# Kernel optimization log

Hardware: AMD Instinct MI355X
Metric: run time of the kernel (lower is better)

Reference implementation:

```python
import math
import jax, jax.numpy as jnp
import numpy as np

NLAT, NLON = 61, 120
C, H = 64, 4
DH = C // H
HID = 128
NSEG = NLAT * NLON  # number of grid points / softmax segments
EPS = 1e-6
SCALE = 1.0 / math.sqrt(DH)


def _build_geometry():
    """Neighbor pairs within theta_cutoff on the equiangular (pole-including) grid.

    The neighborhood structure is longitude-shift invariant, so we enumerate it
    for output longitude 0 and replicate with a modular longitude shift.
    """
    nlat, nlon = NLAT, NLON
    theta = np.pi * np.arange(nlat) / (nlat - 1)           # colatitudes incl. poles
    lam = 2.0 * np.pi * np.arange(nlon) / nlon
    theta_cutoff = 7.0 / math.sqrt(math.pi) * math.pi / (nlat - 1)
    ct, st = np.cos(theta), np.sin(theta)
    # great-circle distance between (theta_o, 0) and (theta_i, dlon): [nlat, nlat, nlon]
    cosd = (ct[:, None, None] * ct[None, :, None]
            + st[:, None, None] * st[None, :, None] * np.cos(lam)[None, None, :])
    dist = np.arccos(np.clip(cosd, -1.0, 1.0))
    ho, hi, dl = np.nonzero(dist <= theta_cutoff)          # E reference-column entries
    wo = np.arange(nlon)
    out_idx = (ho[:, None] * nlon + wo[None, :]).reshape(-1).astype(np.int32)
    in_idx = (hi[:, None] * nlon + (dl[:, None] + wo[None, :]) % nlon).reshape(-1).astype(np.int32)
    # quadrature (integration) weights: sin(theta) measure, zero at the poles
    w = (st * (np.pi / (nlat - 1)) * (2.0 * np.pi / nlon)).astype(np.float32)
    quad_w = np.repeat(w, nlon)                            # [NSEG]
    return jnp.asarray(out_idx), jnp.asarray(in_idx), jnp.asarray(quad_w)


def setup_inputs() -> dict:
    key = jax.random.key(0)
    ks = jax.random.split(key, 8)
    out_idx, in_idx, quad_w = _build_geometry()

    def w(k, shape, fan_in):
        return jax.random.normal(k, shape, dtype=jnp.float32) / np.float32(np.sqrt(fan_in))

    return {
        "x": jax.random.normal(ks[0], (1, C, NLAT, NLON), dtype=jnp.float32),
        "wq": w(ks[1], (C, C), C),
        "wk": w(ks[2], (C, C), C),
        "wv": w(ks[3], (C, C), C),
        "wo": w(ks[4], (C, C), C),
        "w1": w(ks[5], (HID, C), C),
        "b1": jnp.zeros((HID,), jnp.float32),
        "w2": w(ks[6], (C, HID), HID),
        "b2": jnp.zeros((C,), jnp.float32),
        "ln0_g": jnp.ones((C,), jnp.float32),
        "ln0_b": jnp.zeros((C,), jnp.float32),
        "ln1_g": jnp.ones((C,), jnp.float32),
        "ln1_b": jnp.zeros((C,), jnp.float32),
        "quad_w": quad_w,
        "out_idx": out_idx,
        "in_idx": in_idx,
    }


def _layernorm(x, g, b):
    # channel-wise LayerNorm at every spatial location; x: [B, C, H, W]
    m = jnp.mean(x, axis=1, keepdims=True)
    v = jnp.mean((x - m) ** 2, axis=1, keepdims=True)
    xh = (x - m) * jax.lax.rsqrt(v + EPS)
    return xh * g[None, :, None, None] + b[None, :, None, None]


def _neighborhood_attn(x, wq, wk, wv, wo, quad_w, out_idx, in_idx):
    # x: [B, C, nlat, nlon] (fp32)
    B = x.shape[0]
    q = jnp.einsum('oc,bchw->bohw', wq, x).reshape(B, H, DH, NSEG)
    k = jnp.einsum('oc,bchw->bohw', wk, x).reshape(B, H, DH, NSEG)
    v = jnp.einsum('oc,bchw->bohw', wv, x).reshape(B, H, DH, NSEG)
    qg = q[..., out_idx]                                   # [B,H,DH,NNZ]
    kg = k[..., in_idx]
    s = jnp.einsum('bhdn,bhdn->bhn', qg, kg) * SCALE       # [B,H,NNZ]
    s = jnp.moveaxis(s, -1, 0)                             # [NNZ,B,H]
    smax = jax.ops.segment_max(s, out_idx, num_segments=NSEG)
    # quadrature-weighted, numerically stable softmax over each neighborhood
    alpha = jnp.exp(s - smax[out_idx]) * quad_w[in_idx][:, None, None]
    vg = jnp.moveaxis(v[..., in_idx], -1, 0)               # [NNZ,B,H,DH]
    num = jax.ops.segment_sum(alpha[..., None] * vg, out_idx, num_segments=NSEG)
    den = jax.ops.segment_sum(alpha, out_idx, num_segments=NSEG)
    att = num / den[..., None]                             # [NSEG,B,H,DH]
    att = jnp.moveaxis(att, 0, -1).reshape(B, C, NLAT, NLON)
    return jnp.einsum('oc,bchw->bohw', wo, att)


def reference(x, wq, wk, wv, wo, w1, b1, w2, b2, ln0_g, ln0_b, ln1_g, ln1_b,
              quad_w, out_idx, in_idx):
    residual = x
    h0 = _layernorm(x, ln0_g, ln0_b)
    a = _neighborhood_attn(h0.astype(jnp.float32), wq, wk, wv, wo,
                           quad_w, out_idx, in_idx).astype(x.dtype)
    x1 = a + residual
    h1 = _layernorm(x1, ln1_g, ln1_b)
    m = jax.nn.gelu(jnp.einsum('fc,bchw->bfhw', w1, h1) + b1[None, :, None, None],
                    approximate=False)
    m = jnp.einsum('cf,bfhw->bchw', w2, m) + b2[None, :, None, None]
    return m + x1
```

## Files before the change

### kernel.cpp

```cpp
#include <hip/hip_runtime.h>
#include <math.h>

#define NSEG 7320
#define NLON 120
#define HIDN 128
#define ECH  16
#define MAXCH 48

__global__ __launch_bounds__(64) void k1_ln_qkv(
    const float* __restrict__ x,  const float* __restrict__ wq,
    const float* __restrict__ wk, const float* __restrict__ wv,
    const float* __restrict__ g,  const float* __restrict__ b,
    const int* __restrict__ out_idx, const int* __restrict__ in_idx,
    const float* __restrict__ qw, int E,
    float* __restrict__ q_pl, float* __restrict__ k_pl, float* __restrict__ v_pl,
    int* __restrict__ row_start, int4* __restrict__ meta,
    float4* __restrict__ zbase)
{
    const int lane = threadIdx.x;
    const int tile = blockIdx.x;
    const int grp  = blockIdx.y;

    if (grp >= 25) {
        const int n4 = (68 * NSEG) / 4;
        for (int i = ((grp - 25) * 115 + tile) * 64 + lane; i < n4; i += 2 * 115 * 64)
            zbase[i] = make_float4(0.f, 0.f, 0.f, 0.f);
        return;
    }
    if (grp == 24) {
        for (int e = tile * 64 + lane; e < E; e += 115 * 64) {
            int ho = out_idx[e * NLON] / NLON;
            if (e == 0) {
                row_start[ho] = 0;
            } else {
                int hp = out_idx[(e - 1) * NLON] / NLON;
                if (hp != ho) row_start[ho] = e;
            }
            if (e == E - 1) row_start[ho + 1] = E;
            int i0 = in_idx[e * NLON];
            int hi = i0 / NLON;
            int dl = i0 - hi * NLON;
            meta[e] = make_int4(hi * NLON, dl, __float_as_int(qw[i0]), ho);
        }
        return;
    }

    const int n = tile * 64 + lane;
    if (n >= NSEG) return;

    float xv[64];
    float s = 0.f, s2 = 0.f;
#pragma unroll
    for (int c = 0; c < 64; ++c) { float t = x[c * NSEG + n]; xv[c] = t; s += t; s2 += t * t; }
    float mean = s * 0.015625f;
    float var  = s2 * 0.015625f - mean * mean;
    float rstd = rsqrtf(var + 1e-6f);
#pragma unroll
    for (int c = 0; c < 64; ++c) xv[c] = (xv[c] - mean) * rstd * g[c] + b[c];

    const int mm    = grp >> 3;
    const int obase = (grp & 7) * 8;
    const float* __restrict__ w = (mm == 0) ? wq : (mm == 1) ? wk : wv;
    float* __restrict__ dst = (mm == 0) ? q_pl : (mm == 1) ? k_pl : v_pl;
    const float scale = (mm == 0) ? 0.25f : 1.0f;

#pragma unroll
    for (int j = 0; j < 8; ++j) {
        int o = obase + j;
        float acc = 0.f;
#pragma unroll
        for (int c = 0; c < 64; ++c) acc += w[o * 64 + c] * xv[c];
        dst[o * NSEG + n] = acc * scale;
    }
}

__global__ __launch_bounds__(128) void k2_attn(
    const float* __restrict__ q_pl, const float* __restrict__ k_pl,
    const float* __restrict__ v_pl,
    const int4* __restrict__ meta,  const int* __restrict__ row_start,
    float* __restrict__ num, float* __restrict__ den)
{
    const int wo  = threadIdx.x;
    const bool aw = wo < NLON;
    const int woc = aw ? wo : (NLON - 1);
    const int ho  = blockIdx.x;
    const int head = blockIdx.z;
    const int cb  = head * 16;

    int e0 = __builtin_amdgcn_readfirstlane(row_start[ho]);
    int e1 = __builtin_amdgcn_readfirstlane(row_start[ho + 1]);
    int eb = e0 + blockIdx.y * ECH;
    if (eb >= e1) return;
    int ee = eb + ECH; if (ee > e1) ee = e1;

    const int segc = ho * NLON + woc;
    const float* __restrict__ qb = q_pl + (size_t)cb * NSEG;
    const float* __restrict__ kb = k_pl + (size_t)cb * NSEG;
    const float* __restrict__ vb = v_pl + (size_t)cb * NSEG;

    float qreg[16];
#pragma unroll
    for (int c = 0; c < 16; ++c) qreg[c] = qb[c * NSEG + segc];

    float acc[16];
#pragma unroll
    for (int c = 0; c < 16; ++c) acc[c] = 0.f;
    float dh = 0.f;

#pragma unroll 2
    for (int e = eb; e < ee; ++e) {
        int4 mt = meta[e];
        int dlw = mt.y + woc; if (dlw >= NLON) dlw -= NLON;
        const float* __restrict__ kp = kb + (mt.x + dlw);
        const float* __restrict__ vp = vb + (mt.x + dlw);

        float sa = 0.f, sb = 0.f;
#pragma unroll
        for (int c = 0; c < 8; ++c)  sa += qreg[c]     * kp[c * NSEG];
#pragma unroll
        for (int c = 0; c < 8; ++c)  sb += qreg[8 + c] * kp[(8 + c) * NSEG];

        float qwv = aw ? __int_as_float(mt.z) : 0.f;
        float a = __expf(sa + sb) * qwv;
        dh += a;

#pragma unroll
        for (int c = 0; c < 16; ++c) acc[c] = fmaf(a, vp[c * NSEG], acc[c]);
    }

    if (aw) {
        const int seg = ho * NLON + wo;
#pragma unroll
        for (int c = 0; c < 16; ++c) atomicAdd(&num[(cb + c) * NSEG + seg], acc[c]);
        atomicAdd(&den[head * NSEG + seg], dh);
    }
}

__global__ __launch_bounds__(64) void k2c_wo(
    const float* __restrict__ num, const float* __restrict__ den,
    const float* __restrict__ wo,  const float* __restrict__ x,
    float* __restrict__ x1)
{
    const int lane = threadIdx.x;
    const int n    = blockIdx.x * 64 + lane;
    if (n >= NSEG) return;

    float rdh[4];
#pragma unroll
    for (int h = 0; h < 4; ++h) rdh[h] = 1.0f / den[h * NSEG + n];

    float att[64];
#pragma unroll
    for (int c = 0; c < 64; ++c) att[c] = num[c * NSEG + n] * rdh[c >> 4];

    const int o0 = blockIdx.y * 8;
#pragma unroll
    for (int j = 0; j < 8; ++j) {
        int o = o0 + j;
        float acc = 0.f;
#pragma unroll
        for (int c = 0; c < 64; ++c) acc += wo[o * 64 + c] * att[c];
        x1[o * NSEG + n] = acc + x[o * NSEG + n];
    }
}

__global__ __launch_bounds__(64) void k3a_mlp1(
    const float* __restrict__ x1, const float* __restrict__ w1,
    const float* __restrict__ b1, const float* __restrict__ g,
    const float* __restrict__ bb, float* __restrict__ m_act)
{
    const int lane = threadIdx.x;
    const int n    = blockIdx.x * 64 + lane;
    if (n >= NSEG) return;

    float xv[64];
    float s = 0.f, s2 = 0.f;
#pragma unroll
    for (int c = 0; c < 64; ++c) { float t = x1[c * NSEG + n]; xv[c] = t; s += t; s2 += t * t; }
    float mean = s * 0.015625f;
    float var  = s2 * 0.015625f - mean * mean;
    float rstd = rsqrtf(var + 1e-6f);
#pragma unroll
    for (int c = 0; c < 64; ++c) xv[c] = (xv[c] - mean) * rstd * g[c] + bb[c];

    const int h0 = blockIdx.y * 8;
#pragma unroll
    for (int j = 0; j < 8; ++j) {
        int h = h0 + j;
        float mh = b1[h];
#pragma unroll
        for (int c = 0; c < 64; ++c) mh += w1[h * 64 + c] * xv[c];
        m_act[h * NSEG + n] = 0.5f * mh * (1.0f + erff(mh * 0.70710678118654752f));
    }
}

__global__ __launch_bounds__(64) void k3b_mlp2(
    const float* __restrict__ m_act, const float* __restrict__ w2,
    const float* __restrict__ b2,    const float* __restrict__ x1,
    float* __restrict__ out)
{
    const int lane = threadIdx.x;
    const int n    = blockIdx.x * 64 + lane;
    if (n >= NSEG) return;
    const int c0   = blockIdx.y * 8;

    float acc[8];
#pragma unroll
    for (int j = 0; j < 8; ++j) acc[j] = 0.f;

#pragma unroll 8
    for (int h = 0; h < HIDN; ++h) {
        float mh = m_act[h * NSEG + n];
#pragma unroll
        for (int j = 0; j < 8; ++j) acc[j] += w2[(c0 + j) * HIDN + h] * mh;
    }
#pragma unroll
    for (int j = 0; j < 8; ++j) {
        int c = c0 + j;
        out[c * NSEG + n] = acc[j] + b2[c] + x1[c * NSEG + n];
    }
}

extern "C" void kernel_launch(void* const* d_in, const int* in_sizes, int n_in,
                              void* d_out, int out_size, void* d_ws, size_t ws_size,
                              hipStream_t stream)
{
    const float* x    = (const float*)d_in[0];
    const float* wq   = (const float*)d_in[1];
    const float* wk   = (const float*)d_in[2];
    const float* wv   = (const float*)d_in[3];
    const float* wo   = (const float*)d_in[4];
    const float* w1   = (const float*)d_in[5];
    const float* b1   = (const float*)d_in[6];
    const float* w2   = (const float*)d_in[7];
    const float* b2   = (const float*)d_in[8];
    const float* ln0g = (const float*)d_in[9];
    const float* ln0b = (const float*)d_in[10];
    const float* ln1g = (const float*)d_in[11];
    const float* ln1b = (const float*)d_in[12];
    const float* qw   = (const float*)d_in[13];
    const int* out_idx = (const int*)d_in[14];
    const int* in_idx  = (const int*)d_in[15];
    float* out = (float*)d_out;

    const int NNZ = in_sizes[15];
    const int E   = NNZ / NLON;
    const size_t N64 = (size_t)NSEG * 64;

    float* ws    = (float*)d_ws;
    float* q_pl  = ws;
    float* k_pl  = ws + N64;
    float* v_pl  = ws + 2 * N64;
    float* num   = ws + 3 * N64;
    float* den   = ws + 4 * N64;
    float* x1    = ws + 4 * N64 + 4 * NSEG;
    float* m_act = ws + 5 * N64 + 4 * NSEG;
    int*   row_start = (int*)(ws + 7 * N64 + 4 * NSEG);
    int4*  meta  = (int4*)(ws + 7 * N64 + 4 * NSEG + 64);

    hipLaunchKernelGGL(k1_ln_qkv, dim3(115, 27), dim3(64), 0, stream,
                       x, wq, wk, wv, ln0g, ln0b, out_idx, in_idx, qw, E,
                       q_pl, k_pl, v_pl, row_start, meta, (float4*)num);
    hipLaunchKernelGGL(k2_attn, dim3(61, MAXCH, 4), dim3(128), 0, stream,
                       q_pl, k_pl, v_pl, meta, row_start, num, den);
    hipLaunchKernelGGL(k2c_wo, dim3(115, 8), dim3(64), 0, stream,
                       num, den, wo, x, x1);
    hipLaunchKernelGGL(k3a_mlp1, dim3(115, 16), dim3(64), 0, stream,
                       x1, w1, b1, ln1g, ln1b, m_act);
    hipLaunchKernelGGL(k3b_mlp2, dim3(115, 8), dim3(64), 0, stream,
                       m_act, w2, b2, x1, out);
}
```

Before: 186.8 us.

## Replace attention atomics with per-chunk partial buffers and a separate reduction kernel

The attention kernel now writes each edge-chunk's partial numerator and denominator to a dedicated slice of a partial buffer instead of issuing atomicAdds into num/den. A new reduction kernel sums the valid chunks per row, which also removes the need to zero num/den inside the first kernel. The edge chunk size is doubled and the chunk count halved, so there are fewer blocks and fewer partial slices to reduce. This avoids atomic contention and the zeroing pass, at the cost of an extra kernel launch and extra global memory traffic for the partials.

```diff
diff --git a/kernel.cpp b/kernel.cpp
--- a/kernel.cpp
+++ b/kernel.cpp
@@ -4,8 +4,8 @@
 #define NSEG 7320
 #define NLON 120
 #define HIDN 128
-#define ECH  16
-#define MAXCH 48
+#define ECH  32
+#define MAXCH 24
 
 __global__ __launch_bounds__(64) void k1_ln_qkv(
     const float* __restrict__ x,  const float* __restrict__ wq,
@@ -14,19 +14,12 @@
     const int* __restrict__ out_idx, const int* __restrict__ in_idx,
     const float* __restrict__ qw, int E,
     float* __restrict__ q_pl, float* __restrict__ k_pl, float* __restrict__ v_pl,
-    int* __restrict__ row_start, int4* __restrict__ meta,
-    float4* __restrict__ zbase)
+    int* __restrict__ row_start, int4* __restrict__ meta)
 {
     const int lane = threadIdx.x;
     const int tile = blockIdx.x;
     const int grp  = blockIdx.y;
 
-    if (grp >= 25) {
-        const int n4 = (68 * NSEG) / 4;
-        for (int i = ((grp - 25) * 115 + tile) * 64 + lane; i < n4; i += 2 * 115 * 64)
-            zbase[i] = make_float4(0.f, 0.f, 0.f, 0.f);
-        return;
-    }
     if (grp == 24) {
         for (int e = tile * 64 + lane; e < E; e += 115 * 64) {
             int ho = out_idx[e * NLON] / NLON;
@@ -78,18 +71,19 @@
     const float* __restrict__ q_pl, const float* __restrict__ k_pl,
     const float* __restrict__ v_pl,
     const int4* __restrict__ meta,  const int* __restrict__ row_start,
-    float* __restrict__ num, float* __restrict__ den)
+    float* __restrict__ part)
 {
     const int wo  = threadIdx.x;
     const bool aw = wo < NLON;
     const int woc = aw ? wo : (NLON - 1);
     const int ho  = blockIdx.x;
+    const int j   = blockIdx.y;
     const int head = blockIdx.z;
     const int cb  = head * 16;
 
     int e0 = __builtin_amdgcn_readfirstlane(row_start[ho]);
     int e1 = __builtin_amdgcn_readfirstlane(row_start[ho + 1]);
-    int eb = e0 + blockIdx.y * ECH;
+    int eb = e0 + j * ECH;
     if (eb >= e1) return;
     int ee = eb + ECH; if (ee > e1) ee = e1;
 
@@ -130,10 +124,42 @@
 
     if (aw) {
         const int seg = ho * NLON + wo;
-#pragma unroll
-        for (int c = 0; c < 16; ++c) atomicAdd(&num[(cb + c) * NSEG + seg], acc[c]);
-        atomicAdd(&den[head * NSEG + seg], dh);
-    }
+        float* __restrict__ pb = part + ((size_t)j * 68) * NSEG;
+#pragma unroll
+        for (int c = 0; c < 16; ++c)
+            pb[(cb + c) * NSEG + seg] = acc[c];
+        pb[(64 + head) * NSEG + seg] = dh;
+    }
+}
+
+__global__ __launch_bounds__(64) void k2r_reduce(
+    const float* __restrict__ part, const int* __restrict__ row_start,
+    float* __restrict__ num, float* __restrict__ den)
+{
+    const int lane = threadIdx.x;
+    const int n    = blockIdx.x * 64 + lane;
+    if (n >= NSEG) return;
+    const int c    = blockIdx.y;
+    const int row  = n / NLON;
+    const int len  = row_start[row + 1] - row_start[row];
+    const int nch  = (len + ECH - 1) / ECH;
+
+    const float* __restrict__ pb = part + (size_t)c * NSEG + n;
+    const size_t jst = (size_t)68 * NSEG;
+
+    float s0 = 0.f, s1 = 0.f, s2 = 0.f, s3 = 0.f;
+    int j = 0;
+    for (; j + 4 <= nch; j += 4) {
+        s0 += pb[(size_t)j * jst];
+        s1 += pb[(size_t)(j + 1) * jst];
+        s2 += pb[(size_t)(j + 2) * jst];
+        s3 += pb[(size_t)(j + 3) * jst];
+    }
+    for (; j < nch; ++j) s0 += pb[(size_t)j * jst];
+    float s = (s0 + s1) + (s2 + s3);
+
+    if (c < 64) num[c * NSEG + n] = s;
+    else        den[(c - 64) * NSEG + n] = s;
 }
 
 __global__ __launch_bounds__(64) void k2c_wo(
@@ -257,12 +283,15 @@
     float* m_act = ws + 5 * N64 + 4 * NSEG;
     int*   row_start = (int*)(ws + 7 * N64 + 4 * NSEG);
     int4*  meta  = (int4*)(ws + 7 * N64 + 4 * NSEG + 64);
-
-    hipLaunchKernelGGL(k1_ln_qkv, dim3(115, 27), dim3(64), 0, stream,
+    float* part  = ws + 7 * N64 + 4 * NSEG + 64 + 4 * 10240;
+
+    hipLaunchKernelGGL(k1_ln_qkv, dim3(115, 25), dim3(64), 0, stream,
                        x, wq, wk, wv, ln0g, ln0b, out_idx, in_idx, qw, E,
-                       q_pl, k_pl, v_pl, row_start, meta, (float4*)num);
+                       q_pl, k_pl, v_pl, row_start, meta);
     hipLaunchKernelGGL(k2_attn, dim3(61, MAXCH, 4), dim3(128), 0, stream,
-                       q_pl, k_pl, v_pl, meta, row_start, num, den);
+                       q_pl, k_pl, v_pl, meta, row_start, part);
+    hipLaunchKernelGGL(k2r_reduce, dim3(115, 68), dim3(64), 0, stream,
+                       part, row_start, num, den);
     hipLaunchKernelGGL(k2c_wo, dim3(115, 8), dim3(64), 0, stream,
                        num, den, wo, x, x1);
     hipLaunchKernelGGL(k3a_mlp1, dim3(115, 16), dim3(64), 0, stream,
```

Result: slower. 199.2 us (+6.6%).
